# Kernel optimization log

Measured on AMD Instinct MI355X. Metric: run time of the kernel, lower is better.

Reference implementation:

```python
import jax, jax.numpy as jnp
import numpy as np

B, T, H, F_OUT, ATTN_LEN = 8, 2000, 256, 257, 128


def setup_inputs() -> dict:
    key = jax.random.key(0)
    ks = jax.random.split(key, 7)
    s = 1.0 / np.sqrt(H)
    s2 = 1.0 / np.sqrt(2 * H)
    return {
        "k": jax.random.normal(ks[0], (B, T, H), dtype=jnp.float32),
        "q": jax.random.normal(ks[1], (B, T, H), dtype=jnp.float32),
        "W_score": jax.random.uniform(ks[2], (H, H), jnp.float32, -s, s),
        "W_enh": jax.random.uniform(ks[3], (H, 2 * H), jnp.float32, -s2, s2),
        "b_enh": jax.random.uniform(ks[4], (H,), jnp.float32, -s2, s2),
        "W_mask": jax.random.uniform(ks[5], (F_OUT, H), jnp.float32, -s, s),
        "b_mask": jax.random.uniform(ks[6], (F_OUT,), jnp.float32, -s, s),
    }


def reference(k, q, W_score, W_enh, b_enh, W_mask, b_mask):
    # scored query: q @ W_score^T  (torch Linear, no bias)
    qs = jnp.einsum("bth,gh->btg", q, W_score)
    # dense scores [B, T, T]: row t attends over source positions s
    attn_score = jnp.einsum("bth,bsh->bts", qs, k)
    # NOTE: max is taken over the FULL row BEFORE banding (faithful to source)
    attn_max = jnp.max(attn_score, axis=-1, keepdims=True)
    exp_score = jnp.exp(attn_score - attn_max)
    # causal band: tril then triu(diagonal=-attn_len) -> keep t-attn_len <= s <= t
    t_idx = jnp.arange(T)[:, None]
    s_idx = jnp.arange(T)[None, :]
    band = (s_idx <= t_idx) & (s_idx >= t_idx - ATTN_LEN)
    attn_weights = jnp.where(band[None], exp_score, 0.0)
    denom = jnp.sum(attn_weights, axis=-1, keepdims=True)
    attn_weights = attn_weights / (denom + 1e-30)
    c = jnp.einsum("bts,bsh->bth", attn_weights, k)
    out = jnp.concatenate([c, q], axis=-1)  # [B, T, 2H]
    out = jnp.tanh(out @ W_enh.T + b_enh)
    mask_vector = jax.nn.sigmoid(out @ W_mask.T + b_mask)  # [B, T, F_OUT]
    return mask_vector
```

## Files before the change

### kernel.cpp

```cpp
#include <hip/hip_runtime.h>
#include <math.h>

#define B_    8
#define T_    2000
#define H_    256
#define FOUT_ 257
#define ALEN_ 128

typedef __attribute__((ext_vector_type(8))) short bf16x8;
typedef __attribute__((ext_vector_type(4))) float f32x4;
typedef __attribute__((ext_vector_type(8))) unsigned short u16x8;

__device__ __forceinline__ unsigned short f2bf(float x) {
    unsigned u = __builtin_bit_cast(unsigned, x);
    return (unsigned short)((u + 0x7FFFu + ((u >> 16) & 1u)) >> 16);
}
__device__ __forceinline__ void split1(float x, unsigned short& h, unsigned short& l) {
    unsigned u = __builtin_bit_cast(unsigned, x);
    h = (unsigned short)(u >> 16);
    float hf = __builtin_bit_cast(float, u & 0xFFFF0000u);
    l = (unsigned short)(__builtin_bit_cast(unsigned, x - hf) >> 16);
}
__device__ __forceinline__ void split8(float4 f0, float4 f1, bf16x8& h, bf16x8& l) {
    float f[8] = {f0.x, f0.y, f0.z, f0.w, f1.x, f1.y, f1.z, f1.w};
#pragma unroll
    for (int i = 0; i < 8; ++i) {
        unsigned short hh, ll;
        split1(f[i], hh, ll);
        h[i] = (short)hh; l[i] = (short)ll;
    }
}
__device__ __forceinline__ void rne8(float4 f0, float4 f1, bf16x8& h) {
    float f[8] = {f0.x, f0.y, f0.z, f0.w, f1.x, f1.y, f1.z, f1.w};
#pragma unroll
    for (int i = 0; i < 8; ++i) h[i] = (short)f2bf(f[i]);
}
__device__ __forceinline__ void gld16(const void* g, void* l) {
    __builtin_amdgcn_global_load_lds(
        (const __attribute__((address_space(1))) unsigned*)g,
        (__attribute__((address_space(3))) unsigned*)l, 16, 0, 0);
}


__global__ __launch_bounds__(256) void prep(
    const float* __restrict__ k,
    const float* __restrict__ Ws, const float* __restrict__ We,
    const float* __restrict__ Wm,
    unsigned short* __restrict__ kfh, unsigned short* __restrict__ kfl,
    unsigned short* __restrict__ ktn,
    unsigned short* __restrict__ wsnh, unsigned short* __restrict__ wsnl,
    unsigned short* __restrict__ wenh,
    unsigned short* __restrict__ wmnh)
{
    __shared__ float tile[16][260];
    const int bx = blockIdx.x, tid = threadIdx.x;

    if (bx < 1008) {
        const int bid = bx;
        const int b = bid / 126;
        const int g = bid % 126;
        const int s0 = g * 16;
        const int r = tid >> 4, cs = (tid & 15) * 16;
        const int s = s0 + r;
        if (s < T_) {
            const float* src = k + ((size_t)b * T_ + s) * H_ + cs;
#pragma unroll
            for (int i = 0; i < 2; ++i) {
                const float4 v0 = *(const float4*)(src + i * 8);
                const float4 v1 = *(const float4*)(src + i * 8 + 4);
                bf16x8 h, l;
                split8(v0, v1, h, l);
                const int kcol = cs + i * 8;
                const size_t off = ((((size_t)(b * 125 + g) * 8 + (kcol >> 5)) * 4 +
                                     ((kcol >> 3) & 3)) * 16 + r) * 8;
                *(bf16x8*)(kfh + off) = h;
                *(bf16x8*)(kfl + off) = l;
                const float ff[8] = {v0.x, v0.y, v0.z, v0.w, v1.x, v1.y, v1.z, v1.w};
#pragma unroll
                for (int j = 0; j < 8; ++j) tile[r][cs + i * 8 + j] = ff[j];
            }
        } else {
#pragma unroll
            for (int i = 0; i < 16; ++i) tile[r][cs + i] = 0.f;
        }
        __syncthreads();
        const int h = tid;
        const int ht = h >> 4, lq = h & 15;
        u16x8 o0, o1;
#pragma unroll
        for (int ss = 0; ss < 8; ++ss)
            o0[ss] = (unsigned short)(__builtin_bit_cast(unsigned, tile[ss][h]) >> 16);
#pragma unroll
        for (int ss = 0; ss < 8; ++ss)
            o1[ss] = (unsigned short)(__builtin_bit_cast(unsigned, tile[ss + 8][h]) >> 16);
        unsigned short* dst = ktn + (((size_t)(b * 16 + ht) * 126) + g) * 256 + lq * 8;
        *(u16x8*)(dst) = o0;
        *(u16x8*)(dst + 128) = o1;
    } else if (bx < 1264) {
        const int g = bx - 1008;
        const int kk = tid;
        unsigned short h, l; split1(Ws[g * 256 + kk], h, l);
        const size_t off = ((((size_t)(g >> 4) * 8 + (kk >> 5)) * 4 +
                             ((kk >> 3) & 3)) * 16 + (g & 15)) * 8 + (kk & 7);
        wsnh[off] = h; wsnl[off] = l;
    } else if (bx < 1776) {
        const int idx = (bx - 1264) * 256 + tid;
        const int col = idx >> 9;
        const int kk = idx & 511;
        unsigned short h, l; split1(We[idx], h, l);
        const size_t off = ((((size_t)(col >> 4) * 16 + (kk >> 5)) * 4 +
                             ((kk >> 3) & 3)) * 16 + (col & 15)) * 8 + (kk & 7);
        wenh[off] = h;
    } else {
        const int col = bx - 1776;
        if (col < 320) {
            const int kk = tid;
            const float x = (col < FOUT_) ? Wm[col * 256 + kk] : 0.f;
            unsigned short h, l; split1(x, h, l);
            const size_t off = ((((size_t)(col >> 4) * 8 + (kk >> 5)) * 4 +
                                 ((kk >> 3) & 3)) * 16 + (col & 15)) * 8 + (kk & 7);
            wmnh[off] = h;
        }
    }
}

__global__ __launch_bounds__(512) void band_attn_mfma(
    const float* __restrict__ qf,
    const unsigned short* __restrict__ wsnh, const unsigned short* __restrict__ wsnl,
    const unsigned short* __restrict__ kfh, const unsigned short* __restrict__ kfl,
    const unsigned short* __restrict__ ktn,
    unsigned short* __restrict__ Ch)
{
    __shared__ float S[32][164];
    __shared__ unsigned short PH[32][168];
    __shared__ unsigned short PL[32][168];
    __shared__ unsigned short QSH[32 * 256];
    __shared__ unsigned short QSL[32 * 256];

    const int bid = blockIdx.x;
    const int b = bid & 7;
    const int t0 = (bid >> 3) * 32;
    const int tid = threadIdx.x;
    const int w = tid >> 6, l = tid & 63;
    const int sub = w & 1;
    const int wp = w >> 1;
    const int lq = l & 15;
    const int lk = l >> 4;
    const int s_lo = max(0, t0 - ALEN_);
    const int srow = sub * 16;

    {
        const int qr = min(t0 + srow + lq, T_ - 1);
        const float* qp = qf + ((size_t)b * T_ + qr) * H_ + lk * 8;
        bf16x8 aH[8], aL[8];
#pragma unroll
        for (int kg = 0; kg < 8; ++kg) {
            const float4 f0 = *(const float4*)(qp + kg * 32);
            const float4 f1 = *(const float4*)(qp + kg * 32 + 4);
            split8(f0, f1, aH[kg], aL[kg]);
        }
        for (int ht = wp; ht < 16; ht += 4) {
            f32x4 acc = {};
#pragma unroll
            for (int kg = 0; kg < 8; ++kg) {
                const size_t fo = ((size_t)(ht * 8 + kg)) * 1024 + (size_t)l * 16;
                const bf16x8 bh = *(const bf16x8*)((const char*)wsnh + fo);
                const bf16x8 bl = *(const bf16x8*)((const char*)wsnl + fo);
                acc = __builtin_amdgcn_mfma_f32_16x16x32_bf16(aH[kg], bh, acc, 0, 0, 0);
                acc = __builtin_amdgcn_mfma_f32_16x16x32_bf16(aH[kg], bl, acc, 0, 0, 0);
                acc = __builtin_amdgcn_mfma_f32_16x16x32_bf16(aL[kg], bh, acc, 0, 0, 0);
            }
#pragma unroll
            for (int r = 0; r < 4; ++r) {
                unsigned short h2, l2;
                split1(acc[r], h2, l2);
                const int t = srow + lk * 4 + r;
                unsigned off = (unsigned)(t * 512 + (ht * 16 + lq) * 2);
                off ^= (unsigned)((t & 7) << 4);
                *(unsigned short*)((char*)QSH + off) = h2;
                *(unsigned short*)((char*)QSL + off) = l2;
            }
        }
    }
    __syncthreads();

    {
        bf16x8 aH[8], aL[8];
#pragma unroll
        for (int hc = 0; hc < 8; ++hc) {
            const int t = srow + lq;
            unsigned off = (unsigned)(t * 512 + hc * 64 + lk * 16);
            off ^= (unsigned)((t & 7) << 4);
            aH[hc] = *(const bf16x8*)((const char*)QSH + off);
            aL[hc] = *(const bf16x8*)((const char*)QSL + off);
        }
        const int slo16 = s_lo >> 4;
        for (int st = wp; st < 10; st += 4) {
            f32x4 acc = {};
            const int rtk = b * 125 + slo16 + st;
#pragma unroll
            for (int hc = 0; hc < 8; ++hc) {
                const size_t ob = ((size_t)(rtk * 8 + hc)) * 1024 + (size_t)l * 16;
                const bf16x8 bh = *(const bf16x8*)((const char*)kfh + ob);
                const bf16x8 bl = *(const bf16x8*)((const char*)kfl + ob);
                acc = __builtin_amdgcn_mfma_f32_16x16x32_bf16(aH[hc], bh, acc, 0, 0, 0);
                acc = __builtin_amdgcn_mfma_f32_16x16x32_bf16(aH[hc], bl, acc, 0, 0, 0);
                acc = __builtin_amdgcn_mfma_f32_16x16x32_bf16(aL[hc], bh, acc, 0, 0, 0);
            }
#pragma unroll
            for (int r = 0; r < 4; ++r)
                S[srow + lk * 4 + r][st * 16 + lq] = acc[r];
        }
    }
    __syncthreads();

    {
        const int qq = tid >> 4, li = tid & 15;
        const int t = t0 + qq;
        const int jlo = max(0, t - ALEN_) - s_lo;
        const int jhi = t - s_lo;
        float m = -INFINITY;
#pragma unroll
        for (int j = 0; j < 10; ++j) {
            const int s = li + j * 16;
            if (s >= jlo && s <= jhi) m = fmaxf(m, S[qq][s]);
        }
#pragma unroll
        for (int off = 8; off; off >>= 1) m = fmaxf(m, __shfl_xor(m, off));
        float sum = 0.f;
#pragma unroll
        for (int j = 0; j < 10; ++j) {
            const int s = li + j * 16;
            const float e = (s >= jlo && s <= jhi) ? expf(S[qq][s] - m) : 0.f;
            S[qq][s] = e;
            sum += e;
        }
#pragma unroll
        for (int off = 8; off; off >>= 1) sum += __shfl_xor(sum, off);
        const float inv = 1.f / (sum + 1e-30f);
#pragma unroll
        for (int j = 0; j < 10; ++j) {
            const int s = li + j * 16;
            unsigned short hh2, ll2;
            split1(S[qq][s] * inv, hh2, ll2);
            PH[qq][s] = hh2;
            PL[qq][s] = ll2;
        }
    }
    __syncthreads();

    const int gbase = s_lo >> 4;
    for (int ht = wp; ht < 16; ht += 4) {
        f32x4 acc = {};
        const unsigned short* ktb = ktn + ((size_t)(b * 16 + ht) * 126) * 256;
#pragma unroll
        for (int sc = 0; sc < 5; ++sc) {
            const bf16x8 ph = *(const bf16x8*)((const char*)&PH[srow + lq][0] + sc * 64 + lk * 16);
            const bf16x8 pl = *(const bf16x8*)((const char*)&PL[srow + lq][0] + sc * 64 + lk * 16);
            const bf16x8 bt = *(const bf16x8*)(
                ktb + (size_t)(gbase + 2 * sc + (lk >> 1)) * 256 + (lk & 1) * 128 + lq * 8);
            acc = __builtin_amdgcn_mfma_f32_16x16x32_bf16(ph, bt, acc, 0, 0, 0);
            acc = __builtin_amdgcn_mfma_f32_16x16x32_bf16(pl, bt, acc, 0, 0, 0);
        }
        const int rt_c = b * 125 + ((t0 + srow) >> 4);
        const size_t base = (((size_t)rt_c * 8 + (ht >> 1)) * 4 +
                             ((ht & 1) * 2 + (lq >> 3))) * 16;
#pragma unroll
        for (int r = 0; r < 4; ++r) {
            const int trow = t0 + srow + lk * 4 + r;
            if (trow < T_) {
                const size_t o = (base + (lk * 4 + r)) * 8 + (lq & 7);
                Ch[o] = f2bf(acc[r]);
            }
        }
    }
}

__global__ __launch_bounds__(512) void gemm_fused(
    const unsigned short* __restrict__ ch,
    const float* __restrict__ qf,
    const unsigned short* __restrict__ wenh,
    const float* __restrict__ b_enh,
    const unsigned short* __restrict__ wmnh,
    const float* __restrict__ b_mask, float* __restrict__ out)
{
    __shared__ char LDSB[64 * 1024];

    const int bid = blockIdx.x;
    const int tid = threadIdx.x;
    const int w = tid >> 6, l = tid & 63;
    const int lq = l & 15, lk = l >> 4;

#pragma unroll
    for (int p = 0; p < 4; ++p) {
        const size_t D = ((size_t)p * 512 + tid) * 16;
        gld16((const char*)ch + (size_t)bid * 32768 + D, LDSB + D);
    }
#pragma unroll
    for (int p = 0; p < 4; ++p) {
        const int off8 = p * 512 + tid;
        const int rr = off8 & 15, qq = (off8 >> 4) & 3;
        const int kf = (off8 >> 6) & 7, rtl = off8 >> 9;
        const float* src = qf + ((size_t)(bid * 64 + rtl * 16 + rr)) * H_ + kf * 32 + qq * 8;
        const float4 f0 = *(const float4*)(src);
        const float4 f1 = *(const float4*)(src + 4);
        bf16x8 h;
        rne8(f0, f1, h);
        *(bf16x8*)(LDSB + 32768 + (size_t)off8 * 16) = h;
    }
    __syncthreads();

    f32x4 acc[4][2] = {};
    const int ct0 = 2 * w, ct1 = 2 * w + 1;
#pragma unroll
    for (int ph = 0; ph < 2; ++ph) {
        const char* Ah = LDSB + ph * 32768;
#pragma unroll
        for (int kf = 0; kf < 8; ++kf) {
            const size_t bo0 = ((size_t)(ct0 * 16 + ph * 8 + kf)) * 1024 + (size_t)l * 16;
            const size_t bo1 = ((size_t)(ct1 * 16 + ph * 8 + kf)) * 1024 + (size_t)l * 16;
            const bf16x8 bh0 = *(const bf16x8*)((const char*)wenh + bo0);
            const bf16x8 bh1 = *(const bf16x8*)((const char*)wenh + bo1);
#pragma unroll
            for (int rt = 0; rt < 4; ++rt) {
                const size_t ao = ((size_t)(rt * 8 + kf)) * 1024 + (size_t)l * 16;
                const bf16x8 ah = *(const bf16x8*)(Ah + ao);
                acc[rt][0] = __builtin_amdgcn_mfma_f32_16x16x32_bf16(ah, bh0, acc[rt][0], 0, 0, 0);
                acc[rt][1] = __builtin_amdgcn_mfma_f32_16x16x32_bf16(ah, bh1, acc[rt][1], 0, 0, 0);
            }
        }
    }
    __syncthreads();

    {
        char* EH = LDSB;
#pragma unroll
        for (int cc = 0; cc < 2; ++cc) {
            const int col = (2 * w + cc) * 16 + lq;
            const float bv = b_enh[col];
#pragma unroll
            for (int rt = 0; rt < 4; ++rt) {
#pragma unroll
                for (int r = 0; r < 4; ++r) {
                    const int row = rt * 16 + lk * 4 + r;
                    unsigned off = (unsigned)(row * 512 + col * 2);
                    off ^= (unsigned)((row & 7) << 4);
                    *(unsigned short*)(EH + off) = f2bf(tanhf(acc[rt][cc][r] + bv));
                }
            }
        }
    }
    __syncthreads();

    {
        const char* EH = LDSB;
        f32x4 o2[4][3] = {};
#pragma unroll
        for (int kf = 0; kf < 8; ++kf) {
            bf16x8 bh[3];
#pragma unroll
            for (int i = 0; i < 3; ++i) {
                const int ct = w + 8 * i;
                if (ct < 20) {
                    const size_t bo = ((size_t)(ct * 8 + kf)) * 1024 + (size_t)l * 16;
                    bh[i] = *(const bf16x8*)((const char*)wmnh + bo);
                }
            }
#pragma unroll
            for (int rt = 0; rt < 4; ++rt) {
                const int trow = rt * 16 + lq;
                unsigned aoff = (unsigned)(trow * 512 + kf * 64 + lk * 16);
                aoff ^= (unsigned)((trow & 7) << 4);
                const bf16x8 ah = *(const bf16x8*)(EH + aoff);
#pragma unroll
                for (int i = 0; i < 3; ++i) {
                    const int ct = w + 8 * i;
                    if (ct < 20) {
                        o2[rt][i] = __builtin_amdgcn_mfma_f32_16x16x32_bf16(ah, bh[i], o2[rt][i], 0, 0, 0);
                    }
                }
            }
        }
#pragma unroll
        for (int i = 0; i < 3; ++i) {
            const int ct = w + 8 * i;
            if (ct < 20) {
                const int col = ct * 16 + lq;
                if (col < FOUT_) {
                    const float bv = b_mask[col];
#pragma unroll
                    for (int rt = 0; rt < 4; ++rt) {
#pragma unroll
                        for (int r = 0; r < 4; ++r) {
                            const int row = bid * 64 + rt * 16 + lk * 4 + r;
                            out[(size_t)row * FOUT_ + col] =
                                1.f / (1.f + expf(-(o2[rt][i][r] + bv)));
                        }
                    }
                }
            }
        }
    }
}

extern "C" void kernel_launch(void* const* d_in, const int* in_sizes, int n_in,
                              void* d_out, int out_size, void* d_ws, size_t ws_size,
                              hipStream_t stream)
{
    const float* k       = (const float*)d_in[0];
    const float* q       = (const float*)d_in[1];
    const float* W_score = (const float*)d_in[2];
    const float* W_enh   = (const float*)d_in[3];
    const float* b_enh   = (const float*)d_in[4];
    const float* W_mask  = (const float*)d_in[5];
    const float* b_mask  = (const float*)d_in[6];
    float* out = (float*)d_out;

    const size_t MH = (size_t)B_ * T_ * H_;
    unsigned short* ch  = (unsigned short*)d_ws;
    unsigned short* kfh = ch + MH;
    unsigned short* kfl = kfh + MH;
    unsigned short* ktn = kfl + MH;
    unsigned short* wsnh = ktn + (size_t)B_ * 16 * 126 * 256;
    unsigned short* wsnl = wsnh + 65536;
    unsigned short* wenh = wsnl + 65536;
    unsigned short* wmnh = wenh + 131072;

    dim3 blk(256);

    prep<<<dim3(2288), blk, 0, stream>>>(
        k, W_score, W_enh, W_mask,
        kfh, kfl, ktn, wsnh, wsnl, wenh, wmnh);

    band_attn_mfma<<<dim3(504), dim3(512), 0, stream>>>(
        q, wsnh, wsnl, kfh, kfl, ktn, ch);

    gemm_fused<<<dim3(250), dim3(512), 0, stream>>>(
        ch, q, wenh, b_enh, wmnh, b_mask, out);
}
```

Measured before the change: 67.56 us.

## Double query rows per attention block and overlay LDS buffers

```diff
diff --git a/kernel.cpp b/kernel.cpp
--- a/kernel.cpp
+++ b/kernel.cpp
@@ -124,26 +124,22 @@
     }
 }
 
-__global__ __launch_bounds__(512) void band_attn_mfma(
+__global__ __launch_bounds__(1024, 1) void band_attn_mfma(
     const float* __restrict__ qf,
     const unsigned short* __restrict__ wsnh, const unsigned short* __restrict__ wsnl,
     const unsigned short* __restrict__ kfh, const unsigned short* __restrict__ kfl,
     const unsigned short* __restrict__ ktn,
     unsigned short* __restrict__ Ch)
 {
-    __shared__ float S[32][164];
-    __shared__ unsigned short PH[32][168];
-    __shared__ unsigned short PL[32][168];
-    __shared__ unsigned short QSH[32 * 256];
-    __shared__ unsigned short QSL[32 * 256];
+    __shared__ char LDSB[114 * 1024];
 
     const int bid = blockIdx.x;
     const int b = bid & 7;
-    const int t0 = (bid >> 3) * 32;
+    const int t0 = (bid >> 3) * 64;
     const int tid = threadIdx.x;
     const int w = tid >> 6, l = tid & 63;
-    const int sub = w & 1;
-    const int wp = w >> 1;
+    const int sub = w & 3;
+    const int wp = w >> 2;
     const int lq = l & 15;
     const int lk = l >> 4;
     const int s_lo = max(0, t0 - ALEN_);
@@ -177,8 +173,8 @@
                 const int t = srow + lk * 4 + r;
                 unsigned off = (unsigned)(t * 512 + (ht * 16 + lq) * 2);
                 off ^= (unsigned)((t & 7) << 4);
-                *(unsigned short*)((char*)QSH + off) = h2;
-                *(unsigned short*)((char*)QSL + off) = l2;
+                *(unsigned short*)(LDSB + off) = h2;
+                *(unsigned short*)(LDSB + 32768 + off) = l2;
             }
         }
     }
@@ -191,11 +187,11 @@
             const int t = srow + lq;
             unsigned off = (unsigned)(t * 512 + hc * 64 + lk * 16);
             off ^= (unsigned)((t & 7) << 4);
-            aH[hc] = *(const bf16x8*)((const char*)QSH + off);
-            aL[hc] = *(const bf16x8*)((const char*)QSL + off);
+            aH[hc] = *(const bf16x8*)(LDSB + off);
+            aL[hc] = *(const bf16x8*)(LDSB + 32768 + off);
         }
         const int slo16 = s_lo >> 4;
-        for (int st = wp; st < 10; st += 4) {
+        for (int st = wp; st < 12; st += 4) {
             f32x4 acc = {};
             const int rtk = b * 125 + slo16 + st;
 #pragma unroll
@@ -208,8 +204,10 @@
                 acc = __builtin_amdgcn_mfma_f32_16x16x32_bf16(aL[hc], bh, acc, 0, 0, 0);
             }
 #pragma unroll
-            for (int r = 0; r < 4; ++r)
-                S[srow + lk * 4 + r][st * 16 + lq] = acc[r];
+            for (int r = 0; r < 4; ++r) {
+                const int row = srow + lk * 4 + r;
+                *(float*)(LDSB + 65536 + ((size_t)row * 196 + st * 16 + lq) * 4) = acc[r];
+            }
         }
     }
     __syncthreads();
@@ -219,32 +217,35 @@
         const int t = t0 + qq;
         const int jlo = max(0, t - ALEN_) - s_lo;
         const int jhi = t - s_lo;
+        const char* Srow = LDSB + 65536 + (size_t)qq * 784;
         float m = -INFINITY;
 #pragma unroll
-        for (int j = 0; j < 10; ++j) {
+        for (int j = 0; j < 12; ++j) {
             const int s = li + j * 16;
-            if (s >= jlo && s <= jhi) m = fmaxf(m, S[qq][s]);
+            if (s >= jlo && s <= jhi) m = fmaxf(m, *(const float*)(Srow + s * 4));
         }
 #pragma unroll
         for (int off = 8; off; off >>= 1) m = fmaxf(m, __shfl_xor(m, off));
         float sum = 0.f;
-#pragma unroll
-        for (int j = 0; j < 10; ++j) {
+        float ev[12];
+#pragma unroll
+        for (int j = 0; j < 12; ++j) {
             const int s = li + j * 16;
-            const float e = (s >= jlo && s <= jhi) ? expf(S[qq][s] - m) : 0.f;
-            S[qq][s] = e;
+            const float e = (s >= jlo && s <= jhi)
+                ? expf(*(const float*)(Srow + s * 4) - m) : 0.f;
+            ev[j] = e;
             sum += e;
         }
 #pragma unroll
         for (int off = 8; off; off >>= 1) sum += __shfl_xor(sum, off);
         const float inv = 1.f / (sum + 1e-30f);
 #pragma unroll
-        for (int j = 0; j < 10; ++j) {
+        for (int j = 0; j < 12; ++j) {
             const int s = li + j * 16;
             unsigned short hh2, ll2;
-            split1(S[qq][s] * inv, hh2, ll2);
-            PH[qq][s] = hh2;
-            PL[qq][s] = ll2;
+            split1(ev[j] * inv, hh2, ll2);
+            *(unsigned short*)(LDSB + (size_t)qq * 400 + s * 2) = hh2;
+            *(unsigned short*)(LDSB + 25600 + (size_t)qq * 400 + s * 2) = ll2;
         }
     }
     __syncthreads();
@@ -253,10 +254,12 @@
     for (int ht = wp; ht < 16; ht += 4) {
         f32x4 acc = {};
         const unsigned short* ktb = ktn + ((size_t)(b * 16 + ht) * 126) * 256;
-#pragma unroll
-        for (int sc = 0; sc < 5; ++sc) {
-            const bf16x8 ph = *(const bf16x8*)((const char*)&PH[srow + lq][0] + sc * 64 + lk * 16);
-            const bf16x8 pl = *(const bf16x8*)((const char*)&PL[srow + lq][0] + sc * 64 + lk * 16);
+        const char* PHrow = LDSB + (size_t)(srow + lq) * 400;
+        const char* PLrow = LDSB + 25600 + (size_t)(srow + lq) * 400;
+#pragma unroll
+        for (int sc = 0; sc < 6; ++sc) {
+            const bf16x8 ph = *(const bf16x8*)(PHrow + sc * 64 + lk * 16);
+            const bf16x8 pl = *(const bf16x8*)(PLrow + sc * 64 + lk * 16);
             const bf16x8 bt = *(const bf16x8*)(
                 ktb + (size_t)(gbase + 2 * sc + (lk >> 1)) * 256 + (lk & 1) * 128 + lq * 8);
             acc = __builtin_amdgcn_mfma_f32_16x16x32_bf16(ph, bt, acc, 0, 0, 0);
@@ -432,7 +435,7 @@
         k, W_score, W_enh, W_mask,
         kfh, kfl, ktn, wsnh, wsnl, wenh, wmnh);
 
-    band_attn_mfma<<<dim3(504), dim3(512), 0, stream>>>(
+    band_attn_mfma<<<dim3(256), dim3(1024), 0, stream>>>(
         q, wsnh, wsnl, kfh, kfl, ktn, ch);
 
     gemm_fused<<<dim3(250), dim3(512), 0, stream>>>(
```

Result: slower. 69.16 us (+2.4%).
